# Performance work log

Measured on AMD Instinct MI355X. Metric: run time of the kernel, lower is better.

## Reference

```python
import jax, jax.numpy as jnp
import numpy as np

EPS_ATTN = 1e-6
EPS_LN = 1e-5  # torch nn.LayerNorm default eps
NHEAD = 8
L, D, DFF, S, B = 4, 512, 1024, 4096, 8


def _layernorm(x, g, b):
    m = jnp.mean(x, axis=-1, keepdims=True)
    v = jnp.mean((x - m) ** 2, axis=-1, keepdims=True)
    return (x - m) * jax.lax.rsqrt(v + EPS_LN) * g + b


def _layer(src, Wq, bq, Wk, bk, Wv, bv, Wo, bo, g1, be1, W1, bf1, W2, bf2, g2, be2):
    # src: (S, B, D)
    s, b, d = src.shape
    dk = d // NHEAD
    Q = (src @ Wq + bq).reshape(s, b, NHEAD, dk)
    K = (src @ Wk + bk).reshape(s, b, NHEAD, dk)
    V = (src @ Wv + bv).reshape(s, b, NHEAD, dk)
    # ELU+1 feature-map linear attention, vectorized over heads
    phiQ = jax.nn.elu(Q) + 1.0
    phiK = jax.nn.elu(K) + 1.0
    context = jnp.einsum('sbhd,sbhe->bhde', phiK, V)          # (B,H,dk,dk)
    out = jnp.einsum('sbhd,bhde->sbhe', phiQ, context)        # (S,B,H,dk)
    denom = jnp.einsum('sbhd,bhd->sbh', phiQ, phiK.sum(0))    # (S,B,H)
    out = out / (denom[..., None] + EPS_ATTN)
    attn = out.reshape(s, b, d)  # concat heads (same order as torch cat)
    out = attn @ Wo + bo
    out = _layernorm(src + out, g1, be1)
    ffn = jax.nn.relu(out @ W1 + bf1) @ W2 + bf2
    return _layernorm(out + ffn, g2, be2)


def setup_inputs() -> dict:
    key = jax.random.key(0)
    ks = jax.random.split(key, 8)
    sc = 0.02
    inp = {
        'src': jax.random.normal(ks[0], (S, B, D), jnp.float32),
        'Wq': jax.random.normal(ks[1], (L, D, D), jnp.float32) * sc,
        'bq': jnp.zeros((L, D), jnp.float32),
        'Wk': jax.random.normal(ks[2], (L, D, D), jnp.float32) * sc,
        'bk': jnp.zeros((L, D), jnp.float32),
        'Wv': jax.random.normal(ks[3], (L, D, D), jnp.float32) * sc,
        'bv': jnp.zeros((L, D), jnp.float32),
        'Wo': jax.random.normal(ks[4], (L, D, D), jnp.float32) * sc,
        'bo': jnp.zeros((L, D), jnp.float32),
        'ln1_g': jnp.ones((L, D), jnp.float32),
        'ln1_b': jnp.zeros((L, D), jnp.float32),
        'W1': jax.random.normal(ks[5], (L, D, DFF), jnp.float32) * sc,
        'b1': jnp.zeros((L, DFF), jnp.float32),
        'W2': jax.random.normal(ks[6], (L, DFF, D), jnp.float32) * sc,
        'b2': jnp.zeros((L, D), jnp.float32),
        'ln2_g': jnp.ones((L, D), jnp.float32),
        'ln2_b': jnp.zeros((L, D), jnp.float32),
    }
    return inp


def reference(src, Wq, bq, Wk, bk, Wv, bv, Wo, bo, ln1_g, ln1_b, W1, b1, W2, b2, ln2_g, ln2_b):
    x = src
    for i in range(Wq.shape[0]):  # small fixed layer count
        x = _layer(x, Wq[i], bq[i], Wk[i], bk[i], Wv[i], bv[i], Wo[i], bo[i],
                   ln1_g[i], ln1_b[i], W1[i], b1[i], W2[i], b2[i], ln2_g[i], ln2_b[i])
    return x
```

## Files before the change

### kernel.cpp

```cpp
#include <hip/hip_runtime.h>
#include <hip/hip_bf16.h>
#include <cstdint>

typedef __attribute__((ext_vector_type(8))) short short8;
typedef __attribute__((ext_vector_type(4))) float f32x4;
typedef __attribute__((ext_vector_type(4))) unsigned short ushort4v;

#define DEV static __device__ __forceinline__

DEV float bf2f(unsigned short u) {
    union { unsigned int i; float f; } v; v.i = ((unsigned int)u) << 16; return v.f;
}
DEV unsigned short f2bf(float f) {
    union { float f; unsigned int i; } v; v.f = f;
    unsigned int x = v.i;
    unsigned int r = x + 0x7fffu + ((x >> 16) & 1u);
    return (unsigned short)(r >> 16);
}

template<int EPI>
__global__ __launch_bounds__(256) void gemm_kernel(
    const unsigned short* __restrict__ A, int lda,
    const unsigned short* __restrict__ Bt,
    const float* __restrict__ bias,
    unsigned short* __restrict__ outp, int ldc,
    int nshift, int K)
{
    __shared__ unsigned short lds[128 * 136];
    const int t  = threadIdx.x;
    const int w  = t >> 6, l = t & 63;
    const int wr = w >> 1, wc = w & 1;
    const int lr = l & 15, lg = l >> 4;
    const int bid = blockIdx.x;
    const int j8  = bid & 7, s = bid >> 3;
    const int bx  = j8 * 32 + (s >> nshift);
    const int by  = s & ((1 << nshift) - 1);
    const long tM = (long)bx * 128;
    const long tN = (long)by * 128;

    f32x4 acc[4][4];
#pragma unroll
    for (int i = 0; i < 4; i++)
#pragma unroll
        for (int j = 0; j < 4; j++) acc[i][j] = f32x4{0.f, 0.f, 0.f, 0.f};

    const unsigned short* Ab = A  + tM * lda;
    const unsigned short* Bb = Bt + tN * K;

    for (int kt = 0; kt < K; kt += 64) {
#pragma unroll
        for (int j = 0; j < 4; j++) {
            int c = (w * 4 + j) * 64 + l;
            int row = c >> 3, sc = (c & 7) ^ (row & 7);
            __builtin_amdgcn_global_load_lds(
                (const __attribute__((address_space(1))) void*)(Ab + (long)row * lda + kt + sc * 8),
                (__attribute__((address_space(3))) void*)(lds + (w * 4 + j) * 512),
                16, 0, 0);
        }
#pragma unroll
        for (int j = 0; j < 4; j++) {
            int c = (w * 4 + j) * 64 + l;
            int row = c >> 3, sc = (c & 7) ^ (row & 7);
            __builtin_amdgcn_global_load_lds(
                (const __attribute__((address_space(1))) void*)(Bb + (long)row * K + kt + sc * 8),
                (__attribute__((address_space(3))) void*)(lds + 8192 + (w * 4 + j) * 512),
                16, 0, 0);
        }
        __syncthreads();
#pragma unroll
        for (int kk = 0; kk < 2; kk++) {
            short8 af[4], bfv[4];
#pragma unroll
            for (int mi = 0; mi < 4; mi++) {
                int r  = wr * 64 + mi * 16 + lr;
                int kc = kk * 4 + lg;
                af[mi] = *(const short8*)&lds[r * 64 + ((kc ^ (r & 7)) << 3)];
            }
#pragma unroll
            for (int ni = 0; ni < 4; ni++) {
                int n  = wc * 64 + ni * 16 + lr;
                int kc = kk * 4 + lg;
                bfv[ni] = *(const short8*)&lds[8192 + n * 64 + ((kc ^ (n & 7)) << 3)];
            }
#pragma unroll
            for (int mi = 0; mi < 4; mi++)
#pragma unroll
                for (int ni = 0; ni < 4; ni++)
                    acc[mi][ni] = __builtin_amdgcn_mfma_f32_16x16x32_bf16(
                        af[mi], bfv[ni], acc[mi][ni], 0, 0, 0);
        }
        __syncthreads();
    }

    float bv[4];
#pragma unroll
    for (int ni = 0; ni < 4; ni++) bv[ni] = bias[tN + wc * 64 + ni * 16 + lr];
    const bool doElu = (EPI == 0) && (tN < 512);

#pragma unroll
    for (int mi = 0; mi < 4; mi++)
#pragma unroll
        for (int ni = 0; ni < 4; ni++)
#pragma unroll
            for (int j = 0; j < 4; j++) {
                float v = acc[mi][ni][j] + bv[ni];
                if (EPI == 0) { if (doElu) v = (v > 0.f) ? (v + 1.f) : expf(v); }
                if (EPI == 2) v = fmaxf(v, 0.f);
                int r = wr * 64 + mi * 16 + lg * 4 + j;
                int c = wc * 64 + ni * 16 + lr;
                lds[r * 136 + c] = f2bf(v);
            }
    __syncthreads();
#pragma unroll
    for (int i = 0; i < 8; i++) {
        int q = i * 256 + t;
        int r = q >> 4, cc = q & 15;
        short8 v8 = *(const short8*)&lds[r * 136 + cc * 8];
        *(short8*)&outp[(tM + r) * ldc + tN + cc * 8] = v8;
    }
}

__global__ __launch_bounds__(512) void gemm_ln_kernel(
    const unsigned short* __restrict__ A, int lda,
    const unsigned short* __restrict__ Bt,
    const float* __restrict__ bias,
    const float* __restrict__ res,
    const float* __restrict__ g,
    const float* __restrict__ be,
    float* __restrict__ of,
    unsigned short* __restrict__ ob,
    int K)
{
    __shared__ unsigned short sA[128 * 64];
    __shared__ unsigned short sB[512 * 64];
    float* redb = (float*)sA;
    float* statb = redb + 1024;
    const int t = threadIdx.x, w = t >> 6, l = t & 63, lr = l & 15, lg = l >> 4;
    const int wr = w >> 2, wc = w & 3;
    const long tM = (long)blockIdx.x * 128;

    f32x4 acc[4][8];
#pragma unroll
    for (int i = 0; i < 4; i++)
#pragma unroll
        for (int j = 0; j < 8; j++) acc[i][j] = f32x4{0.f, 0.f, 0.f, 0.f};

    const unsigned short* Ab = A + tM * lda;

    for (int kt = 0; kt < K; kt += 64) {
#pragma unroll
        for (int j = 0; j < 2; j++) {
            int c = j * 512 + t;
            int row = c >> 3, sc = (c & 7) ^ (row & 7);
            __builtin_amdgcn_global_load_lds(
                (const __attribute__((address_space(1))) void*)(Ab + (long)row * lda + kt + sc * 8),
                (__attribute__((address_space(3))) void*)(sA + (j * 512 + w * 64) * 8),
                16, 0, 0);
        }
#pragma unroll
        for (int j = 0; j < 8; j++) {
            int c = j * 512 + t;
            int row = c >> 3, sc = (c & 7) ^ (row & 7);
            __builtin_amdgcn_global_load_lds(
                (const __attribute__((address_space(1))) void*)(Bt + (long)row * K + kt + sc * 8),
                (__attribute__((address_space(3))) void*)(sB + (j * 512 + w * 64) * 8),
                16, 0, 0);
        }
        __syncthreads();
#pragma unroll
        for (int kk = 0; kk < 2; kk++) {
            short8 av[4], bw[8];
#pragma unroll
            for (int mi = 0; mi < 4; mi++) {
                int r = wr * 64 + mi * 16 + lr, kc = kk * 4 + lg;
                av[mi] = *(const short8*)&sA[r * 64 + ((kc ^ (r & 7)) << 3)];
            }
#pragma unroll
            for (int ni = 0; ni < 8; ni++) {
                int n = wc * 128 + ni * 16 + lr, kc = kk * 4 + lg;
                bw[ni] = *(const short8*)&sB[n * 64 + ((kc ^ (n & 7)) << 3)];
            }
#pragma unroll
            for (int mi = 0; mi < 4; mi++)
#pragma unroll
                for (int ni = 0; ni < 8; ni++)
                    acc[mi][ni] = __builtin_amdgcn_mfma_f32_16x16x32_bf16(
                        av[mi], bw[ni], acc[mi][ni], 0, 0, 0);
        }
        __syncthreads();
    }

    float gv[8], bev[8], bb[8];
#pragma unroll
    for (int ni = 0; ni < 8; ni++) {
        int col = wc * 128 + ni * 16 + lr;
        gv[ni] = g[col]; bev[ni] = be[col]; bb[ni] = bias[col];
    }
#pragma unroll
    for (int mi = 0; mi < 4; mi++)
#pragma unroll
        for (int jj = 0; jj < 4; jj++) {
            long row = tM + wr * 64 + mi * 16 + lg * 4 + jj;
#pragma unroll
            for (int ni = 0; ni < 8; ni++) {
                int col = wc * 128 + ni * 16 + lr;
                acc[mi][ni][jj] += bb[ni] + res[row * 512 + col];
            }
        }
    float s2[4][4], ss2[4][4];
#pragma unroll
    for (int mi = 0; mi < 4; mi++)
#pragma unroll
        for (int jj = 0; jj < 4; jj++) {
            float s = 0.f, ss = 0.f;
#pragma unroll
            for (int ni = 0; ni < 8; ni++) {
                float v = acc[mi][ni][jj];
                s += v; ss += v * v;
            }
#pragma unroll
            for (int off = 1; off < 16; off <<= 1) {
                s  += __shfl_xor(s, off);
                ss += __shfl_xor(ss, off);
            }
            s2[mi][jj] = s; ss2[mi][jj] = ss;
        }
    __syncthreads();
    if (lr == 0) {
#pragma unroll
        for (int mi = 0; mi < 4; mi++)
#pragma unroll
            for (int jj = 0; jj < 4; jj++) {
                int rb = wr * 64 + mi * 16 + lg * 4 + jj;
                redb[0 * 512 + wc * 128 + rb] = s2[mi][jj];
                redb[1 * 512 + wc * 128 + rb] = ss2[mi][jj];
            }
    }
    __syncthreads();
    if (t < 128) {
        float S  = redb[t] + redb[128 + t] + redb[256 + t] + redb[384 + t];
        float SS = redb[512 + t] + redb[640 + t] + redb[768 + t] + redb[896 + t];
        float mean = S * (1.0f / 512.0f);
        float var  = SS * (1.0f / 512.0f) - mean * mean;
        statb[t] = mean;
        statb[128 + t] = rsqrtf(fmaxf(var, 0.f) + 1e-5f);
    }
    __syncthreads();
#pragma unroll
    for (int mi = 0; mi < 4; mi++)
#pragma unroll
        for (int jj = 0; jj < 4; jj++) {
            int rb = wr * 64 + mi * 16 + lg * 4 + jj;
            long row = tM + rb;
            float mean = statb[rb], rstd = statb[128 + rb];
#pragma unroll
            for (int ni = 0; ni < 8; ni++) {
                int col = wc * 128 + ni * 16 + lr;
                float y = (acc[mi][ni][jj] - mean) * rstd * gv[ni] + bev[ni];
                of[row * 512 + col] = y;
                ob[row * 512 + col] = f2bf(y);
            }
        }
}

__global__ __launch_bounds__(256) void ctx_partial_kernel(
    const unsigned short* __restrict__ kv, float* __restrict__ part,
    float* __restrict__ part2)
{
    const int p = blockIdx.x, ch = blockIdx.y;
    const int b = p >> 3, h = p & 7;
    __shared__ float kb[64 * 68];
    __shared__ float vbuf[64 * 68];
    const int t = threadIdx.x;
    const int dq = t >> 4, eq = t & 15;
    f32x4 acc[4];
    f32x4 ks = {0.f, 0.f, 0.f, 0.f};
#pragma unroll
    for (int i = 0; i < 4; i++) acc[i] = f32x4{0.f, 0.f, 0.f, 0.f};

    for (int sub = 0; sub < 8; sub++) {
        int sbase = ch * 512 + sub * 64;
#pragma unroll
        for (int i = 0; i < 2; i++) {
            int idx = i * 256 + t;
            int row = idx >> 3, c8 = idx & 7;
            long ga = ((long)(sbase + row) * 8 + b) * 1024 + h * 64 + c8 * 8;
            short8 kvv = *(const short8*)&kv[ga];
            short8 vv  = *(const short8*)&kv[ga + 512];
#pragma unroll
            for (int j = 0; j < 8; j++) {
                kb[row * 68 + c8 * 8 + j]   = bf2f((unsigned short)kvv[j]);
                vbuf[row * 68 + c8 * 8 + j] = bf2f((unsigned short)vv[j]);
            }
        }
        __syncthreads();
        for (int s = 0; s < 64; s++) {
            f32x4 k4 = *(const f32x4*)&kb[s * 68 + dq * 4];
            f32x4 v4 = *(const f32x4*)&vbuf[s * 68 + eq * 4];
#pragma unroll
            for (int i = 0; i < 4; i++) acc[i] += k4[i] * v4;
            ks += k4;
        }
        __syncthreads();
    }
    float* o = part + (long)(p * 8 + ch) * 4096;
#pragma unroll
    for (int i = 0; i < 4; i++)
        *(f32x4*)&o[(dq * 4 + i) * 64 + eq * 4] = acc[i];
    if (eq == 0)
        *(f32x4*)&part2[(p * 8 + ch) * 64 + dq * 4] = ks;
}

__global__ __launch_bounds__(256) void ctx_reduce_kernel(
    const float* __restrict__ part, const float* __restrict__ part2,
    unsigned short* __restrict__ ctxA)
{
    int o = (blockIdx.x * 256 + threadIdx.x) * 4;
    int p = o >> 12, d = (o >> 6) & 63, e0 = o & 63;
    f32x4 s = {0.f, 0.f, 0.f, 0.f};
    for (int ch = 0; ch < 8; ch++)
        s += *(const f32x4*)&part[(long)(p * 8 + ch) * 4096 + d * 64 + e0];
#pragma unroll
    for (int j = 0; j < 4; j++) ctxA[p * 5120 + (e0 + j) * 64 + d] = f2bf(s[j]);
    if (e0 == 0) {
        float ksv = 0.f;
#pragma unroll
        for (int ch = 0; ch < 8; ch++) ksv += part2[(p * 8 + ch) * 64 + d];
        ctxA[p * 5120 + 4096 + d] = f2bf(ksv);
#pragma unroll
        for (int j = 1; j < 16; j++) ctxA[p * 5120 + 4096 + j * 64 + d] = 0;
    }
}

__global__ __launch_bounds__(256) void attn_out_kernel(
    unsigned short* __restrict__ kv,
    const unsigned short* __restrict__ ctxA)
{
    const int p = blockIdx.x;
    const int b = p >> 3, h = p & 7;
    const int t = threadIdx.x, w = t >> 6, l = t & 63, lr = l & 15, lg = l >> 4;
    const int s0 = blockIdx.y * 256 + w * 64;
    f32x4 acc[4][5];
#pragma unroll
    for (int i = 0; i < 4; i++)
#pragma unroll
        for (int j = 0; j < 5; j++) acc[i][j] = f32x4{0.f, 0.f, 0.f, 0.f};
    const unsigned short* cb = ctxA + p * 5120;
#pragma unroll
    for (int kk = 0; kk < 2; kk++) {
        short8 af[4], bfv[5];
#pragma unroll
        for (int mi = 0; mi < 4; mi++) {
            int s = s0 + mi * 16 + lr;
            af[mi] = *(const short8*)&kv[((long)s * 8 + b) * 1024 + 512 + h * 64 + kk * 32 + lg * 8];
        }
#pragma unroll
        for (int ni = 0; ni < 5; ni++)
            bfv[ni] = *(const short8*)&cb[(ni * 16 + lr) * 64 + kk * 32 + lg * 8];
#pragma unroll
        for (int mi = 0; mi < 4; mi++)
#pragma unroll
            for (int ni = 0; ni < 5; ni++)
                acc[mi][ni] = __builtin_amdgcn_mfma_f32_16x16x32_bf16(
                    af[mi], bfv[ni], acc[mi][ni], 0, 0, 0);
    }
#pragma unroll
    for (int mi = 0; mi < 4; mi++) {
#pragma unroll
        for (int j = 0; j < 4; j++) {
            float den = __shfl(acc[mi][4][j], (l & 48));
            float rc  = 1.0f / (den + 1e-6f);
            int s = s0 + mi * 16 + lg * 4 + j;
            long base = ((long)s * 8 + b) * 1024 + h * 64;
#pragma unroll
            for (int ni = 0; ni < 4; ni++)
                kv[base + ni * 16 + lr] = f2bf(acc[mi][ni][j] * rc);
        }
    }
}

__global__ __launch_bounds__(256) void cvtbf_kernel(
    const float* __restrict__ x, unsigned short* __restrict__ y)
{
    long i = ((long)blockIdx.x * 256 + threadIdx.x) * 8;
    f32x4 a = *(const f32x4*)&x[i];
    f32x4 c = *(const f32x4*)&x[i + 4];
    short8 pk;
#pragma unroll
    for (int j = 0; j < 4; j++) { pk[j] = (short)f2bf(a[j]); pk[4 + j] = (short)f2bf(c[j]); }
    *(short8*)&y[i] = pk;
}

__global__ __launch_bounds__(256) void bcat_kernel(
    const float* __restrict__ bk, const float* __restrict__ bv, float* __restrict__ dst)
{
    int lyr = blockIdx.x;
    int j = blockIdx.y * 256 + threadIdx.x;
    dst[lyr * 1024 + j] = (j < 512) ? bk[lyr * 512 + j] : bv[lyr * 512 + j - 512];
}

__global__ __launch_bounds__(256) void wconv_kernel(
    const float* __restrict__ W, unsigned short* __restrict__ Wt, int K, int N,
    long lstrW, long lstrT)
{
    __shared__ float tile[64 * 65];
    const long lz = blockIdx.z;
    const float* Wl = W + lz * lstrW;
    unsigned short* Wtl = Wt + lz * lstrT;
    const int k0 = blockIdx.x * 64, n0 = blockIdx.y * 64;
    const int t = threadIdx.x;
#pragma unroll
    for (int i = 0; i < 4; i++) {
        int q = i * 256 + t;
        int r = q >> 4, c4 = q & 15;
        f32x4 v = *(const f32x4*)&Wl[(long)(k0 + r) * N + n0 + c4 * 4];
#pragma unroll
        for (int j = 0; j < 4; j++) tile[r * 65 + c4 * 4 + j] = v[j];
    }
    __syncthreads();
#pragma unroll
    for (int i = 0; i < 4; i++) {
        int q = i * 256 + t;
        int nr = q >> 4, kc = q & 15;
        ushort4v pk;
#pragma unroll
        for (int j = 0; j < 4; j++) pk[j] = f2bf(tile[(kc * 4 + j) * 65 + nr]);
        *(ushort4v*)&Wtl[(long)(n0 + nr) * K + k0 + kc * 4] = pk;
    }
}

extern "C" void kernel_launch(void* const* d_in, const int* in_sizes, int n_in,
                              void* d_out, int out_size, void* d_ws, size_t ws_size,
                              hipStream_t stream)
{
    const float* src  = (const float*)d_in[0];
    const float* Wq   = (const float*)d_in[1];
    const float* bq   = (const float*)d_in[2];
    const float* Wk   = (const float*)d_in[3];
    const float* bk   = (const float*)d_in[4];
    const float* Wv   = (const float*)d_in[5];
    const float* bv   = (const float*)d_in[6];
    const float* Wo   = (const float*)d_in[7];
    const float* bo   = (const float*)d_in[8];
    const float* l1g  = (const float*)d_in[9];
    const float* l1b  = (const float*)d_in[10];
    const float* W1   = (const float*)d_in[11];
    const float* b1   = (const float*)d_in[12];
    const float* W2   = (const float*)d_in[13];
    const float* b2   = (const float*)d_in[14];
    const float* l2g  = (const float*)d_in[15];
    const float* l2b  = (const float*)d_in[16];

    char* ws = (char*)d_ws;
    constexpr size_t SZ_WKV = (size_t)4 * 1024 * 512 * 2;
    constexpr size_t SZ_WQ  = (size_t)4 * 512 * 512 * 2;
    constexpr size_t SZ_WO  = SZ_WQ;
    constexpr size_t SZ_W1  = (size_t)4 * 512 * 1024 * 2;
    constexpr size_t SZ_W2  = SZ_W1;
    constexpr size_t SZ_BKV = (size_t)4 * 1024 * 4;
    constexpr size_t SZ_R1  = (size_t)32768 * 512 * 2;
    constexpr size_t SZ_KV  = (size_t)32768 * 1024 * 2;
    constexpr size_t OFF_WKV = 0;
    constexpr size_t OFF_WQ  = OFF_WKV + SZ_WKV;
    constexpr size_t OFF_WO  = OFF_WQ + SZ_WQ;
    constexpr size_t OFF_W1  = OFF_WO + SZ_WO;
    constexpr size_t OFF_W2  = OFF_W1 + SZ_W1;
    constexpr size_t OFF_BKV = OFF_W2 + SZ_W2;
    constexpr size_t OFF_R1  = OFF_BKV + SZ_BKV;
    constexpr size_t OFF_KV  = OFF_R1 + SZ_R1;
    constexpr size_t OFF_KSP = OFF_KV + SZ_KV;
    constexpr size_t OFF_CTP = OFF_KSP + (size_t)16 * 4096 * 4;
    constexpr size_t OFF_CTA = OFF_CTP + (size_t)64 * 8 * 4096 * 4;

    unsigned short* WKVT = (unsigned short*)(ws + OFF_WKV);
    unsigned short* WQT  = (unsigned short*)(ws + OFF_WQ);
    unsigned short* WOT  = (unsigned short*)(ws + OFF_WO);
    unsigned short* W1T  = (unsigned short*)(ws + OFF_W1);
    unsigned short* W2T  = (unsigned short*)(ws + OFF_W2);
    float*          BKV  = (float*)(ws + OFF_BKV);
    unsigned short* R1   = (unsigned short*)(ws + OFF_R1);
    unsigned short* KV   = (unsigned short*)(ws + OFF_KV);
    float*          KSP  = (float*)(ws + OFF_KSP);
    float*          CTP  = (float*)(ws + OFF_CTP);
    unsigned short* CTA  = (unsigned short*)(ws + OFF_CTA);
    float*          F1   = (float*)d_out;

    dim3 blk(256);
    wconv_kernel<<<dim3(8, 8, 4),  blk, 0, stream>>>(Wk, WKVT,            512, 512, 512*512, 1024*512);
    wconv_kernel<<<dim3(8, 8, 4),  blk, 0, stream>>>(Wv, WKVT + 512*512,  512, 512, 512*512, 1024*512);
    wconv_kernel<<<dim3(8, 8, 4),  blk, 0, stream>>>(Wq, WQT,             512, 512, 512*512, 512*512);
    wconv_kernel<<<dim3(8, 8, 4),  blk, 0, stream>>>(Wo, WOT,             512, 512, 512*512, 512*512);
    wconv_kernel<<<dim3(8, 16, 4), blk, 0, stream>>>(W1, W1T,             512, 1024, 512*1024, 512*1024);
    wconv_kernel<<<dim3(16, 8, 4), blk, 0, stream>>>(W2, W2T,             1024, 512, 1024*512, 1024*512);
    bcat_kernel<<<dim3(4, 4), blk, 0, stream>>>(bk, bv, BKV);
    cvtbf_kernel<<<8192, blk, 0, stream>>>(src, R1);

    for (int lyr = 0; lyr < 4; lyr++) {
        const unsigned short* wkvt = WKVT + (size_t)lyr * 1024 * 512;
        const unsigned short* wqt  = WQT  + (size_t)lyr * 512 * 512;
        const unsigned short* wot  = WOT  + (size_t)lyr * 512 * 512;
        const unsigned short* w1t  = W1T  + (size_t)lyr * 512 * 1024;
        const unsigned short* w2t  = W2T  + (size_t)lyr * 1024 * 512;

        gemm_kernel<0><<<2048, blk, 0, stream>>>(R1, 512, wkvt, BKV + lyr * 1024, KV, 1024, 3, 512);

        ctx_partial_kernel<<<dim3(64, 8), blk, 0, stream>>>(KV, CTP, KSP);
        ctx_reduce_kernel<<<256, blk, 0, stream>>>(CTP, KSP, CTA);

        gemm_kernel<0><<<1024, blk, 0, stream>>>(R1, 512, wqt, bq + lyr * 512, KV + 512, 1024, 2, 512);
        attn_out_kernel<<<dim3(64, 16), blk, 0, stream>>>(KV, CTA);

        const float* resp = (lyr == 0) ? src : F1;
        gemm_ln_kernel<<<256, dim3(512), 0, stream>>>(KV, 1024, wot, bo + lyr * 512, resp,
                                                      l1g + lyr * 512, l1b + lyr * 512,
                                                      F1, R1, 512);
        gemm_kernel<2><<<2048, blk, 0, stream>>>(R1, 512, w1t, b1 + lyr * 1024, KV, 1024, 3, 512);
        gemm_ln_kernel<<<256, dim3(512), 0, stream>>>(KV, 1024, w2t, b2 + lyr * 512, F1,
                                                      l2g + lyr * 512, l2b + lyr * 512,
                                                      F1, R1, 1024);
    }
}
```

Before: 1.333 ms.

## Double-buffer LDS in fused GEMM+LayerNorm kernel with K-step of 32

The GEMM+LayerNorm kernel now keeps two LDS buffers, each holding a K-slice of 32 instead of one slice of 64. It issues the global-to-LDS loads for the next slice before running the MFMAs on the current one, so there is one barrier per iteration instead of two. The aim is to hide global load latency behind compute. The cost is more loop iterations with half the MFMA work per barrier, plus a new XOR swizzle pattern for the narrower rows.

Result: no change. 1.314 ms (-1.4%).

```diff
diff --git a/kernel.cpp b/kernel.cpp
--- a/kernel.cpp
+++ b/kernel.cpp
@@ -131,9 +131,9 @@
     unsigned short* __restrict__ ob,
     int K)
 {
-    __shared__ unsigned short sA[128 * 64];
-    __shared__ unsigned short sB[512 * 64];
-    float* redb = (float*)sA;
+    __shared__ unsigned short sA[2][128 * 32];
+    __shared__ unsigned short sB[2][512 * 32];
+    float* redb  = (float*)&sA[0][0];
     float* statb = redb + 1024;
     const int t = threadIdx.x, w = t >> 6, l = t & 63, lr = l & 15, lg = l >> 4;
     const int wr = w >> 2, wc = w & 3;
@@ -147,48 +147,54 @@
 
     const unsigned short* Ab = A + tM * lda;
 
-    for (int kt = 0; kt < K; kt += 64) {
-#pragma unroll
-        for (int j = 0; j < 2; j++) {
-            int c = j * 512 + t;
-            int row = c >> 3, sc = (c & 7) ^ (row & 7);
+    auto STAGE = [&](int buf, int kt) {
+        {
+            int c = t, row = c >> 2, sc = (c & 3) ^ ((row >> 1) & 3);
             __builtin_amdgcn_global_load_lds(
                 (const __attribute__((address_space(1))) void*)(Ab + (long)row * lda + kt + sc * 8),
-                (__attribute__((address_space(3))) void*)(sA + (j * 512 + w * 64) * 8),
+                (__attribute__((address_space(3))) void*)(&sA[buf][t * 8]),
                 16, 0, 0);
         }
 #pragma unroll
-        for (int j = 0; j < 8; j++) {
-            int c = j * 512 + t;
-            int row = c >> 3, sc = (c & 7) ^ (row & 7);
+        for (int j = 0; j < 4; j++) {
+            int c = j * 512 + t, row = c >> 2, sc = (c & 3) ^ ((row >> 1) & 3);
             __builtin_amdgcn_global_load_lds(
                 (const __attribute__((address_space(1))) void*)(Bt + (long)row * K + kt + sc * 8),
-                (__attribute__((address_space(3))) void*)(sB + (j * 512 + w * 64) * 8),
+                (__attribute__((address_space(3))) void*)(&sB[buf][c * 8]),
                 16, 0, 0);
         }
+    };
+
+    auto COMPUTE = [&](int buf) {
+        short8 av[4], bw[8];
+#pragma unroll
+        for (int mi = 0; mi < 4; mi++) {
+            int r = wr * 64 + mi * 16 + lr;
+            av[mi] = *(const short8*)&sA[buf][r * 32 + ((lg ^ ((r >> 1) & 3)) << 3)];
+        }
+#pragma unroll
+        for (int ni = 0; ni < 8; ni++) {
+            int n = wc * 128 + ni * 16 + lr;
+            bw[ni] = *(const short8*)&sB[buf][n * 32 + ((lg ^ ((n >> 1) & 3)) << 3)];
+        }
+#pragma unroll
+        for (int mi = 0; mi < 4; mi++)
+#pragma unroll
+            for (int ni = 0; ni < 8; ni++)
+                acc[mi][ni] = __builtin_amdgcn_mfma_f32_16x16x32_bf16(
+                    av[mi], bw[ni], acc[mi][ni], 0, 0, 0);
+    };
+
+    STAGE(0, 0);
+    __syncthreads();
+    int cur = 0;
+    for (int kt = 32; kt < K; kt += 32) {
+        STAGE(cur ^ 1, kt);
+        COMPUTE(cur);
         __syncthreads();
-#pragma unroll
-        for (int kk = 0; kk < 2; kk++) {
-            short8 av[4], bw[8];
-#pragma unroll
-            for (int mi = 0; mi < 4; mi++) {
-                int r = wr * 64 + mi * 16 + lr, kc = kk * 4 + lg;
-                av[mi] = *(const short8*)&sA[r * 64 + ((kc ^ (r & 7)) << 3)];
-            }
-#pragma unroll
-            for (int ni = 0; ni < 8; ni++) {
-                int n = wc * 128 + ni * 16 + lr, kc = kk * 4 + lg;
-                bw[ni] = *(const short8*)&sB[n * 64 + ((kc ^ (n & 7)) << 3)];
-            }
-#pragma unroll
-            for (int mi = 0; mi < 4; mi++)
-#pragma unroll
-                for (int ni = 0; ni < 8; ni++)
-                    acc[mi][ni] = __builtin_amdgcn_mfma_f32_16x16x32_bf16(
-                        av[mi], bw[ni], acc[mi][ni], 0, 0, 0);
-        }
-        __syncthreads();
-    }
+        cur ^= 1;
+    }
+    COMPUTE(cur);
 
     float gv[8], bev[8], bb[8];
 #pragma unroll
```
